# Performance work log

Hardware: AMD Instinct MI355X
Metric: run time of the kernel (lower is better)

The kernel has to match this reference:

```python
import jax, jax.numpy as jnp
from jax import lax
import numpy as np

SIGNAL_DIM = 64
FR_SIZE = 4096
REG = 0.5
MAX_ITER = 25
TOL = 1e-5
BATCH = 1024


def make_dict():
    # D[t, f] = exp(i * 2*pi * f * t), f on grid [-0.5, 0.5) with spacing 1/FR_SIZE
    freq = jnp.arange(-0.5, 0.5, 1.0 / FR_SIZE, dtype=jnp.float32)[None, :]  # [1, F]
    t = jnp.arange(SIGNAL_DIM, dtype=jnp.float32)[:, None]                   # [N, 1]
    return jnp.exp(1j * 2.0 * jnp.pi * freq * t).astype(jnp.complex64)       # [N, F]


def setup_inputs() -> dict:
    key = jax.random.key(0)
    x = jax.random.normal(key, (BATCH, 2, SIGNAL_DIM), dtype=jnp.float32)
    return {"x": x, "D": make_dict()}


def _soft_complex(u, thr):
    # complex soft-threshold: shrink magnitude, keep phase
    mag = jnp.abs(u)
    scale = jnp.where(mag > thr, (mag - thr) / jnp.maximum(mag, 1e-12), 0.0)
    return u * scale.astype(u.dtype)


def reference(x, D):
    xc = (x[:, 0] + 1j * x[:, 1]).astype(jnp.complex64)  # [B, N]
    Dc = jnp.conj(D)                                      # [N, F]
    # D @ D^H = FR_SIZE * I for this oversampled Fourier dictionary,
    # so the Lipschitz constant of the gradient is L = sigma_max(D)^2 = FR_SIZE.
    step = jnp.float32(1.0 / FR_SIZE)
    thr = jnp.float32(REG) * step
    B = xc.shape[0]
    z0 = jnp.zeros((B, FR_SIZE), dtype=jnp.complex64)

    def cond(state):
        z, w, t, k, err = state
        return (k < MAX_ITER) & (err > TOL)

    def body(state):
        z, w, t, k, _ = state
        resid = w @ D.T - xc                 # [B, N]  (= (D z)^T - x)
        g = resid @ Dc                        # [B, F]  (= D^H resid)
        z_new = _soft_complex(w - step * g, thr)
        t_new = (1.0 + jnp.sqrt(1.0 + 4.0 * t * t)) / 2.0
        w_new = z_new + ((t - 1.0) / t_new).astype(jnp.complex64) * (z_new - z)
        err = jnp.linalg.norm(z_new - z) / jnp.maximum(jnp.linalg.norm(z), 1e-12)
        return (z_new, w_new, t_new, k + 1, err.astype(jnp.float32))

    init = (z0, z0, jnp.float32(1.0), jnp.int32(0), jnp.float32(jnp.inf))
    z_final, _, _, _, _ = lax.while_loop(cond, body, init)

    mag = jnp.abs(z_final)                    # [B, F]
    return mag / jnp.max(mag)                 # global-max normalization, as in torch .max()
```

## Files before the change

### kernel.cpp

```cpp
#include <hip/hip_runtime.h>
#include <math.h>

#define FR    4096
#define NSIG  64
#define NITER 25
#define BROWS 1024
#define PAD   258

typedef float v2f __attribute__((ext_vector_type(2)));

__device__ __forceinline__ v2f mk2(float a, float b) { v2f r; r.x = a; r.y = b; return r; }
__device__ __forceinline__ v2f sp(float a) { v2f r; r.x = a; r.y = a; return r; }

__device__ __forceinline__ v2f pk_add(v2f a, v2f b) {
    v2f d; asm("v_pk_add_f32 %0, %1, %2" : "=v"(d) : "v"(a), "v"(b)); return d;
}
__device__ __forceinline__ v2f pk_sub(v2f a, v2f b) {
    v2f d; asm("v_pk_add_f32 %0, %1, %2 neg_lo:[0,1] neg_hi:[0,1]" : "=v"(d) : "v"(a), "v"(b)); return d;
}
__device__ __forceinline__ v2f pk_addi(v2f a, v2f b) {
    v2f d; asm("v_pk_add_f32 %0, %1, %2 op_sel:[0,1] op_sel_hi:[1,0] neg_lo:[0,1] neg_hi:[0,0]"
               : "=v"(d) : "v"(a), "v"(b)); return d;
}
__device__ __forceinline__ v2f pk_subi(v2f a, v2f b) {
    v2f d; asm("v_pk_add_f32 %0, %1, %2 op_sel:[0,1] op_sel_hi:[1,0] neg_lo:[0,0] neg_hi:[0,1]"
               : "=v"(d) : "v"(a), "v"(b)); return d;
}
__device__ __forceinline__ v2f pk_fma_bl(v2f a, v2f b, v2f c) {
    v2f d;
    asm("v_pk_fma_f32 %0, %1, %2, %3 op_sel:[0,0,0] op_sel_hi:[0,1,1]"
        : "=v"(d) : "v"(a), "v"(b), "v"(c));
    return d;
}
__device__ __forceinline__ v2f pk_fmai_bh(v2f a, v2f b, v2f c) {
    v2f d;
    asm("v_pk_fma_f32 %0, %1, %2, %3 op_sel:[1,1,0] op_sel_hi:[1,0,1] neg_lo:[0,1,0]"
        : "=v"(d) : "v"(a), "v"(b), "v"(c));
    return d;
}
__device__ __forceinline__ v2f pk_muli_bh(v2f a, v2f b) {
    v2f d;
    asm("v_pk_mul_f32 %0, %1, %2 op_sel:[1,1] op_sel_hi:[1,0] neg_lo:[0,1]"
        : "=v"(d) : "v"(a), "v"(b));
    return d;
}
__device__ __forceinline__ v2f pk_mul_bl(v2f a, v2f b) {
    v2f d;
    asm("v_pk_mul_f32 %0, %1, %2 op_sel:[0,0] op_sel_hi:[0,1]"
        : "=v"(d) : "v"(a), "v"(b));
    return d;
}
__device__ __forceinline__ v2f cfma(v2f a, v2f b, v2f c) {
    return pk_fma_bl(a, b, pk_fmai_bh(a, b, c));
}
__device__ __forceinline__ v2f cmul(v2f a, v2f b) {
    return pk_fma_bl(a, b, pk_muli_bh(a, b));
}

__global__ void init_ws(unsigned* g) { *g = 0u; }

template<int S>
__device__ __forceinline__ void dft16p(v2f* X) {
    v2f s[4][4];
    #pragma unroll
    for (int r = 0; r < 4; ++r) {
        v2f a0 = X[r], a1 = X[r + 4], a2 = X[r + 8], a3 = X[r + 12];
        v2f b0 = pk_add(a0, a2), b1 = pk_sub(a0, a2);
        v2f b2 = pk_add(a1, a3), b3 = pk_sub(a1, a3);
        s[r][0] = pk_add(b0, b2);
        s[r][2] = pk_sub(b0, b2);
        if (S > 0) { s[r][1] = pk_addi(b1, b3); s[r][3] = pk_subi(b1, b3); }
        else       { s[r][1] = pk_subi(b1, b3); s[r][3] = pk_addi(b1, b3); }
    }
    const float C1 = 0.9238795325112867f;
    const float S1 = 0.3826834323650898f;
    const float H  = 0.7071067811865476f;
    const float sg = (S > 0) ? 1.0f : -1.0f;
    const v2f K1 = mk2(C1, sg * S1);
    const v2f KH = mk2(H,  sg * H);
    const v2f K3 = mk2(S1, sg * C1);
    #pragma unroll
    for (int p = 0; p < 4; ++p) {
        v2f t0 = s[0][p];
        v2f b0, b1, b2, b3;
        if (p == 0) {
            v2f t1 = s[1][0], t2 = s[2][0], t3 = s[3][0];
            b0 = pk_add(t0, t2); b1 = pk_sub(t0, t2);
            b2 = pk_add(t1, t3); b3 = pk_sub(t1, t3);
        } else if (p == 1) {
            v2f t1 = cmul(s[1][1], K1);
            v2f t2 = cmul(s[2][1], KH);
            v2f t3 = cmul(s[3][1], K3);
            b0 = pk_add(t0, t2); b1 = pk_sub(t0, t2);
            b2 = pk_add(t1, t3); b3 = pk_sub(t1, t3);
        } else if (p == 2) {
            v2f t1 = cmul(s[1][2], KH);
            v2f q3 = cmul(s[3][2], KH);
            if (S > 0) { b0 = pk_addi(t0, s[2][2]); b1 = pk_subi(t0, s[2][2]);
                         b2 = pk_addi(t1, q3);      b3 = pk_subi(t1, q3); }
            else       { b0 = pk_subi(t0, s[2][2]); b1 = pk_addi(t0, s[2][2]);
                         b2 = pk_subi(t1, q3);      b3 = pk_addi(t1, q3); }
        } else {
            v2f t1 = cmul(s[1][3], K3);
            v2f q2 = cmul(s[2][3], KH);
            v2f q3 = cmul(s[3][3], K1);
            if (S > 0) { b0 = pk_addi(t0, q2); b1 = pk_subi(t0, q2); }
            else       { b0 = pk_subi(t0, q2); b1 = pk_addi(t0, q2); }
            b2 = pk_sub(t1, q3); b3 = pk_add(t1, q3);
        }
        X[p]     = pk_add(b0, b2);
        X[p + 8] = pk_sub(b0, b2);
        if (S > 0) { X[p + 4] = pk_addi(b1, b3); X[p + 12] = pk_subi(b1, b3); }
        else       { X[p + 4] = pk_subi(b1, b3); X[p + 12] = pk_addi(b1, b3); }
    }
}

__global__ __launch_bounds__(256) void fista_kernel(const float* __restrict__ x,
                                                    float* __restrict__ out,
                                                    unsigned* __restrict__ gmax)
{
    __shared__ __attribute__((aligned(16))) v2f W_s[16 * PAD];
    __shared__ __attribute__((aligned(16))) v2f resid_s[NSIG];
    __shared__ v2f xc_s[NSIG];
    __shared__ v2f red_s[4][NSIG];
    __shared__ float wmax_s[4];

    const int tid  = (int)threadIdx.x;
    const int lane = tid & 63;
    const int wv   = tid >> 6;
    const int row  = (int)blockIdx.x;

    const float STEP = 1.0f / 4096.0f;
    const float THR  = 0.5f / 4096.0f;

    if (tid < NSIG)
        xc_s[tid] = mk2(x[row * 128 + tid], x[row * 128 + 64 + tid]);

    v2f w[16], zo[16];
    #pragma unroll
    for (int k = 0; k < 16; ++k) { w[k] = sp(0.f); zo[k] = sp(0.f); }

    v2f P0, Rv, R2v, R4v, R8v;
    {
        float sn, cs;
        const float ang0 = (float)M_PI * (float)lane * (float)(wv - 32) * (1.0f / 32.0f);
        sincosf(ang0, &sn, &cs);                                      P0 = mk2(cs, sn);
        sincosf(2.0f * (float)M_PI * (float)lane * (1.0f / 4096.0f), &sn, &cs);
        Rv = mk2(cs, sn);
        R2v = cmul(Rv, Rv);
        R4v = cmul(R2v, R2v);
        R8v = cmul(R4v, R4v);
    }
    v2f Bv, B2v, B3v, Am[16];
    {
        const float td = (float)(tid - 2048);
        float sn, cs;
        v2f Av;
        sincosf(-2.0f * (float)M_PI * td * (1.0f / 4096.0f), &sn, &cs); Av = mk2(cs, sn);
        sincosf(-(float)M_PI * td * (1.0f / 128.0f), &sn, &cs);         Bv = mk2(cs, sn);
        sincosf(-(float)M_PI * td * (1.0f / 64.0f), &sn, &cs);          B2v = mk2(cs, sn);
        sincosf(-3.0f * (float)M_PI * td * (1.0f / 128.0f), &sn, &cs);  B3v = mk2(cs, sn);
        Am[0] = mk2(1.f, 0.f);
        #pragma unroll
        for (int m = 1; m < 16; ++m) Am[m] = cmul(Am[m - 1], Av);
    }

    float tf = 1.0f;

    for (int it = 0; it < NITER; ++it) {
        v2f X[16];
        #pragma unroll
        for (int k = 0; k < 16; ++k) X[k] = w[k];
        dft16p<1>(X);
        #pragma unroll
        for (int m = 0; m < 16; ++m)
            W_s[m * PAD + tid] = X[m];

        {
            v2f acc0 = sp(0.f), acc1 = sp(0.f);
            v2f P = P0;
            const float4* W4 = (const float4*)W_s;
            const int base4 = ((lane & 15) * PAD + wv * 64) >> 1;
            #pragma unroll
            for (int c = 0; c < 8; ++c) {
                float4 a0 = W4[base4 + 4 * c + 0];
                float4 b0 = W4[base4 + 4 * c + 1];
                float4 a1 = W4[base4 + 4 * c + 2];
                float4 b1 = W4[base4 + 4 * c + 3];
                v2f pA = cfma(mk2(a0.z, a0.w), Rv, mk2(a0.x, a0.y));
                v2f pB = cfma(mk2(b0.z, b0.w), Rv, mk2(b0.x, b0.y));
                v2f Wc0 = cfma(pB, R2v, pA);
                acc0 = cfma(Wc0, P, acc0);
                v2f pC = cfma(mk2(a1.z, a1.w), Rv, mk2(a1.x, a1.y));
                v2f pD = cfma(mk2(b1.z, b1.w), Rv, mk2(b1.x, b1.y));
                v2f Wc1 = cfma(pD, R2v, pC);
                acc1 = cfma(Wc1, P, acc1);
                P = cmul(P, R8v);
            }
            red_s[wv][lane] = pk_add(acc0, cmul(acc1, R4v));
        }
        __syncthreads();
        if (tid < NSIG) {
            v2f r = pk_add(pk_add(red_s[0][tid], red_s[1][tid]),
                           pk_add(red_s[2][tid], red_s[3][tid]));
            resid_s[tid] = pk_sub(r, xc_s[tid]);
        }
        __syncthreads();

        v2f g[16];
        {
            const float4* r4 = (const float4*)resid_s;
            #pragma unroll
            for (int mp = 0; mp < 8; ++mp) {
                float4 q0 = r4[mp];
                float4 q1 = r4[mp + 8];
                float4 q2 = r4[mp + 16];
                float4 q3 = r4[mp + 24];
                #pragma unroll
                for (int h = 0; h < 2; ++h) {
                    v2f r0 = h ? mk2(q0.z, q0.w) : mk2(q0.x, q0.y);
                    v2f r1 = h ? mk2(q1.z, q1.w) : mk2(q1.x, q1.y);
                    v2f r2 = h ? mk2(q2.z, q2.w) : mk2(q2.x, q2.y);
                    v2f r3 = h ? mk2(q3.z, q3.w) : mk2(q3.x, q3.y);
                    v2f hA = cfma(r1, Bv, r0);
                    v2f hB = cfma(r3, B3v, cmul(r2, B2v));
                    g[2 * mp + h] = cmul(pk_add(hA, hB), Am[2 * mp + h]);
                }
            }
        }
        dft16p<-1>(g);

        float tn = 0.5f * (1.0f + sqrtf(fmaf(4.0f * tf, tf, 1.0f)));
        float mu = (tf - 1.0f) * __builtin_amdgcn_rcpf(tn);
        tf = tn;
        const v2f nstep = mk2(-STEP, 0.f);
        const v2f muv   = mk2(mu, 0.f);
        #pragma unroll
        for (int k = 0; k < 16; ++k) {
            v2f v = pk_fma_bl(nstep, g[k], w[k]);
            float m2 = fmaf(v.x, v.x, v.y * v.y);
            float q  = __builtin_amdgcn_rsqf(m2);
            float sc = fmaxf(fmaf(-THR, q, 1.0f), 0.0f);
            v2f z = pk_mul_bl(mk2(sc, sc), v);
            v2f d = pk_sub(z, zo[k]);
            w[k] = pk_fma_bl(muv, d, z);
            zo[k] = z;
        }
    }

    float mg[16];
    float lmax = 0.f;
    #pragma unroll
    for (int k = 0; k < 16; ++k) {
        mg[k] = sqrtf(fmaf(zo[k].x, zo[k].x, zo[k].y * zo[k].y));
        lmax = fmaxf(lmax, mg[k]);
    }
    #pragma unroll
    for (int k = 0; k < 16; ++k)
        out[row * FR + k * 256 + tid] = mg[k];

    #pragma unroll
    for (int off = 32; off > 0; off >>= 1)
        lmax = fmaxf(lmax, __shfl_down(lmax, off));
    if (lane == 0) wmax_s[wv] = lmax;
    __syncthreads();
    if (tid == 0) {
        float m4 = fmaxf(fmaxf(wmax_s[0], wmax_s[1]), fmaxf(wmax_s[2], wmax_s[3]));
        atomicMax(gmax, __float_as_uint(m4));
    }
}

__global__ __launch_bounds__(256) void norm_kernel(float4* __restrict__ out,
                                                   const unsigned* __restrict__ gmax)
{
    const float inv = 1.0f / __uint_as_float(*gmax);
    int i = (int)blockIdx.x * 256 + (int)threadIdx.x;
    float4 v = out[i];
    v.x *= inv; v.y *= inv; v.z *= inv; v.w *= inv;
    out[i] = v;
}

extern "C" void kernel_launch(void* const* d_in, const int* in_sizes, int n_in,
                              void* d_out, int out_size, void* d_ws, size_t ws_size,
                              hipStream_t stream)
{
    const float* x = (const float*)d_in[0];
    float* out = (float*)d_out;
    unsigned* gmax = (unsigned*)d_ws;

    init_ws<<<1, 1, 0, stream>>>(gmax);
    fista_kernel<<<BROWS, 256, 0, stream>>>(x, out, gmax);
    norm_kernel<<<(FR * BROWS) / (256 * 4), 256, 0, stream>>>((float4*)out, gmax);
}
```

Before: 191.5 us.

## Store forward-DFT intermediates in LDS as packed bf16 and trim twiddle registers

The per-iteration W matrix written to shared memory is converted to packed bf16 pairs, which halves LDS footprint and read bandwidth in the residual reduction. The LDS pad changes to 260 to fit the new 4-byte layout. The twiddle array Am[16] is cut to 8 even powers, with odd ones computed on the fly, and launch bounds request 6 waves per SIMD to raise occupancy. This trades accuracy (bf16 rounding of the DFT values feeding the residual) and a little extra ALU work for lower LDS traffic and register pressure.

Measured after the change: 673.6 us. +251.8%, slower.

```diff
diff --git a/kernel.cpp b/kernel.cpp
--- a/kernel.cpp
+++ b/kernel.cpp
@@ -5,7 +5,7 @@
 #define NSIG  64
 #define NITER 25
 #define BROWS 1024
-#define PAD   258
+#define PADW  260
 
 typedef float v2f __attribute__((ext_vector_type(2)));
 
@@ -55,6 +55,18 @@
 }
 __device__ __forceinline__ v2f cmul(v2f a, v2f b) {
     return pk_fma_bl(a, b, pk_muli_bh(a, b));
+}
+
+__device__ __forceinline__ unsigned pk_bf16(v2f a) {
+    unsigned d;
+    asm("v_cvt_pk_bf16_f32 %0, %1, %2" : "=v"(d) : "v"(a.y), "v"(a.x));
+    return d;
+}
+__device__ __forceinline__ v2f unp(unsigned u) {
+    v2f r;
+    r.x = __uint_as_float(u & 0xFFFF0000u);
+    r.y = __uint_as_float(u << 16);
+    return r;
 }
 
 __global__ void init_ws(unsigned* g) { *g = 0u; }
@@ -115,11 +127,11 @@
     }
 }
 
-__global__ __launch_bounds__(256) void fista_kernel(const float* __restrict__ x,
-                                                    float* __restrict__ out,
-                                                    unsigned* __restrict__ gmax)
+__global__ __launch_bounds__(256, 6) void fista_kernel(const float* __restrict__ x,
+                                                       float* __restrict__ out,
+                                                       unsigned* __restrict__ gmax)
 {
-    __shared__ __attribute__((aligned(16))) v2f W_s[16 * PAD];
+    __shared__ __attribute__((aligned(16))) unsigned W16[16 * PADW];
     __shared__ __attribute__((aligned(16))) v2f resid_s[NSIG];
     __shared__ v2f xc_s[NSIG];
     __shared__ v2f red_s[4][NSIG];
@@ -151,18 +163,18 @@
         R4v = cmul(R2v, R2v);
         R8v = cmul(R4v, R4v);
     }
-    v2f Bv, B2v, B3v, Am[16];
+    v2f Bv, B2v, B3v, Av, AmE[8];
     {
         const float td = (float)(tid - 2048);
         float sn, cs;
-        v2f Av;
         sincosf(-2.0f * (float)M_PI * td * (1.0f / 4096.0f), &sn, &cs); Av = mk2(cs, sn);
         sincosf(-(float)M_PI * td * (1.0f / 128.0f), &sn, &cs);         Bv = mk2(cs, sn);
         sincosf(-(float)M_PI * td * (1.0f / 64.0f), &sn, &cs);          B2v = mk2(cs, sn);
         sincosf(-3.0f * (float)M_PI * td * (1.0f / 128.0f), &sn, &cs);  B3v = mk2(cs, sn);
-        Am[0] = mk2(1.f, 0.f);
+        v2f A2 = cmul(Av, Av);
+        AmE[0] = mk2(1.f, 0.f);
         #pragma unroll
-        for (int m = 1; m < 16; ++m) Am[m] = cmul(Am[m - 1], Av);
+        for (int m = 1; m < 8; ++m) AmE[m] = cmul(AmE[m - 1], A2);
     }
 
     float tf = 1.0f;
@@ -174,25 +186,25 @@
         dft16p<1>(X);
         #pragma unroll
         for (int m = 0; m < 16; ++m)
-            W_s[m * PAD + tid] = X[m];
+            W16[m * PADW + tid] = pk_bf16(X[m]);
 
         {
             v2f acc0 = sp(0.f), acc1 = sp(0.f);
             v2f P = P0;
-            const float4* W4 = (const float4*)W_s;
-            const int base4 = ((lane & 15) * PAD + wv * 64) >> 1;
+            const uint4* W4 = (const uint4*)W16;
+            const int base4 = ((lane & 15) * PADW + wv * 64) >> 2;
             #pragma unroll
             for (int c = 0; c < 8; ++c) {
-                float4 a0 = W4[base4 + 4 * c + 0];
-                float4 b0 = W4[base4 + 4 * c + 1];
-                float4 a1 = W4[base4 + 4 * c + 2];
-                float4 b1 = W4[base4 + 4 * c + 3];
-                v2f pA = cfma(mk2(a0.z, a0.w), Rv, mk2(a0.x, a0.y));
-                v2f pB = cfma(mk2(b0.z, b0.w), Rv, mk2(b0.x, b0.y));
+                uint4 a = W4[base4 + 2 * c];
+                uint4 b = W4[base4 + 2 * c + 1];
+                v2f W0 = unp(a.x), W1 = unp(a.y), W2 = unp(a.z), W3 = unp(a.w);
+                v2f pA = cfma(W1, Rv, W0);
+                v2f pB = cfma(W3, Rv, W2);
                 v2f Wc0 = cfma(pB, R2v, pA);
                 acc0 = cfma(Wc0, P, acc0);
-                v2f pC = cfma(mk2(a1.z, a1.w), Rv, mk2(a1.x, a1.y));
-                v2f pD = cfma(mk2(b1.z, b1.w), Rv, mk2(b1.x, b1.y));
+                v2f W4v = unp(b.x), W5 = unp(b.y), W6 = unp(b.z), W7 = unp(b.w);
+                v2f pC = cfma(W5, Rv, W4v);
+                v2f pD = cfma(W7, Rv, W6);
                 v2f Wc1 = cfma(pD, R2v, pC);
                 acc1 = cfma(Wc1, P, acc1);
                 P = cmul(P, R8v);
@@ -216,6 +228,8 @@
                 float4 q1 = r4[mp + 8];
                 float4 q2 = r4[mp + 16];
                 float4 q3 = r4[mp + 24];
+                v2f twe = AmE[mp];
+                v2f two = cmul(twe, Av);
                 #pragma unroll
                 for (int h = 0; h < 2; ++h) {
                     v2f r0 = h ? mk2(q0.z, q0.w) : mk2(q0.x, q0.y);
@@ -224,7 +238,7 @@
                     v2f r3 = h ? mk2(q3.z, q3.w) : mk2(q3.x, q3.y);
                     v2f hA = cfma(r1, Bv, r0);
                     v2f hB = cfma(r3, B3v, cmul(r2, B2v));
-                    g[2 * mp + h] = cmul(pk_add(hA, hB), Am[2 * mp + h]);
+                    g[2 * mp + h] = cmul(pk_add(hA, hB), h ? two : twe);
                 }
             }
         }
```
